# Kernel optimization log

Measured on AMD Instinct MI355X. Metric: run time of the kernel, lower is better.

## Reference

```python
import jax, jax.numpy as jnp
import numpy as np

B, S, D, H = 4, 2048, 1024, 16
HD = D // H


def setup_inputs() -> dict:
    key = jax.random.key(0)
    ks = jax.random.split(key, 12)
    s = 1.0 / np.sqrt(D)
    return {
        "query": jax.random.normal(ks[0], (B, S, D), jnp.float32),
        "key_": jax.random.normal(ks[1], (B, S, D), jnp.float32),
        "value": jax.random.normal(ks[2], (B, S, D), jnp.float32),
        "mask": jnp.ones((1, 1, S, S), dtype=bool),
        "Wq": jax.random.normal(ks[3], (D, D), jnp.float32) * s,
        "bq": jnp.zeros((D,), jnp.float32),
        "Wk": jax.random.normal(ks[4], (D, D), jnp.float32) * s,
        "bk": jnp.zeros((D,), jnp.float32),
        "Wv": jax.random.normal(ks[5], (D, D), jnp.float32) * s,
        "bv": jnp.zeros((D,), jnp.float32),
        "Wo": jax.random.normal(ks[6], (D, D), jnp.float32) * s,
        "bo": jnp.zeros((D,), jnp.float32),
    }


def reference(query, key_, value, mask, Wq, bq, Wk, bk, Wv, bv, Wo, bo):
    # Linear projections (torch Linear: x @ W^T + b; here W stored as (in, out))
    Q = query @ Wq + bq   # [B,S,D]
    K = key_ @ Wk + bk
    V = value @ Wv + bv
    # split heads -> [B,H,S,HD]
    Q = Q.reshape(B, S, H, HD).transpose(0, 2, 1, 3)
    K = K.reshape(B, S, H, HD).transpose(0, 2, 1, 3)
    V = V.reshape(B, S, H, HD).transpose(0, 2, 1, 3)
    scores = jnp.einsum("bhqd,bhkd->bhqk", Q, K) / jnp.sqrt(jnp.float32(HD))
    scores = jnp.where(mask, scores, jnp.float32(-jnp.inf))
    attn = jax.nn.softmax(scores, axis=-1)          # [B,H,S,S]
    ctx = jnp.einsum("bhqk,bhkd->bhqd", attn, V)    # dropout = identity (eval)
    ctx = ctx.transpose(0, 2, 1, 3).reshape(B, S, D)
    out = ctx @ Wo + bo
    return out, attn
```

## Files before the change

kernel.cpp:

```cpp
#include <hip/hip_runtime.h>

typedef __attribute__((ext_vector_type(4))) unsigned short u16x4;
typedef __attribute__((ext_vector_type(8))) short short8;
typedef __attribute__((ext_vector_type(4))) short short4b;
typedef __attribute__((ext_vector_type(4))) float f32x4;

__device__ inline unsigned short f2bf(float f) {
    union { float f; unsigned int i; } v; v.f = f;
    unsigned int r = v.i + 0x7fffu + ((v.i >> 16) & 1u);
    return (unsigned short)(r >> 16);
}

#define MFMA_PV(a, b, c) __builtin_amdgcn_mfma_f32_16x16x16bf16_1k((a), (b), (c), 0, 0, 0)
#define MFMA32(a, b, c) __builtin_amdgcn_mfma_f32_16x16x32_bf16((a), (b), (c), 0, 0, 0)

__device__ inline void gload_lds16(const unsigned short* g, unsigned short* l) {
    __builtin_amdgcn_global_load_lds(
        (const __attribute__((address_space(1))) void*)g,
        (__attribute__((address_space(3))) void*)l,
        16, 0, 0);
}

__global__ __launch_bounds__(256) void convert_f32_bf16(const float* __restrict__ in,
                                                        unsigned short* __restrict__ out,
                                                        int n4) {
    int i = blockIdx.x * 256 + threadIdx.x;
    if (i >= n4) return;
    float4 v = ((const float4*)in)[i];
    u16x4 o = { f2bf(v.x), f2bf(v.y), f2bf(v.z), f2bf(v.w) };
    ((u16x4*)out)[i] = o;
}

__global__ __launch_bounds__(256) void transpose_w4(const float* __restrict__ W0,
                                                    const float* __restrict__ W1,
                                                    const float* __restrict__ W2,
                                                    const float* __restrict__ W3,
                                                    unsigned short* __restrict__ O0,
                                                    unsigned short* __restrict__ O1,
                                                    unsigned short* __restrict__ O2,
                                                    unsigned short* __restrict__ O3) {
    __shared__ unsigned short tile[32][33];
    const float* in = (blockIdx.z == 0) ? W0 : (blockIdx.z == 1) ? W1
                    : (blockIdx.z == 2) ? W2 : W3;
    unsigned short* out = (blockIdx.z == 0) ? O0 : (blockIdx.z == 1) ? O1
                        : (blockIdx.z == 2) ? O2 : O3;
    int c0 = blockIdx.x * 32, r0 = blockIdx.y * 32;
    int x = threadIdx.x & 31, y = threadIdx.x >> 5;
#pragma unroll
    for (int i = 0; i < 4; i++)
        tile[y + i * 8][x] = f2bf(in[(size_t)(r0 + y + i * 8) * 1024 + c0 + x]);
    __syncthreads();
#pragma unroll
    for (int i = 0; i < 4; i++)
        out[(size_t)(c0 + y + i * 8) * 1024 + r0 + x] = tile[x][y + i * 8];
}

template <int F32OUT, int KTILED, int VTILED>
__global__ __launch_bounds__(256) void gemm_bt(const unsigned short* __restrict__ X,
                                               const unsigned short* __restrict__ Wt,
                                               const float* __restrict__ bias,
                                               void* __restrict__ outp,
                                               int M, int N, int K) {
    __shared__ unsigned short As[128 * 64];
    __shared__ unsigned short Bs[128 * 64];
    const int t = threadIdx.x;
    const int l = t & 63, w = t >> 6;
    const int lg = l >> 4, ln = l & 15;
    const int wm = (w >> 1) * 64, wn = (w & 1) * 64;
    const int m0 = blockIdx.y * 128, n0 = blockIdx.x * 128;

    const f32x4 zero = {0.f, 0.f, 0.f, 0.f};
    f32x4 acc[4][4];
#pragma unroll
    for (int i = 0; i < 4; i++)
#pragma unroll
        for (int j = 0; j < 4; j++) acc[i][j] = zero;

    int sr[4], sc[4];
#pragma unroll
    for (int i = 0; i < 4; i++) {
        int pos = i * 2048 + t * 8;
        sr[i] = pos >> 6;
        int c8 = (pos >> 3) & 7;
        sc[i] = (c8 ^ (sr[i] & 7)) * 8;
    }

    for (int k0 = 0; k0 < K; k0 += 64) {
#pragma unroll
        for (int i = 0; i < 4; i++)
            gload_lds16(&X[(size_t)(m0 + sr[i]) * K + k0 + sc[i]], &As[i * 2048 + w * 512]);
#pragma unroll
        for (int i = 0; i < 4; i++)
            gload_lds16(&Wt[(size_t)(n0 + sr[i]) * K + k0 + sc[i]], &Bs[i * 2048 + w * 512]);
        __syncthreads();
#pragma unroll
        for (int kk = 0; kk < 2; kk++) {
            short8 af[4], bfr[4];
#pragma unroll
            for (int i = 0; i < 4; i++) {
                int sl = (((kk << 2) | lg) ^ (ln & 7)) * 8;
                af[i]  = *(const short8*)&As[(wm + i * 16 + ln) * 64 + sl];
                bfr[i] = *(const short8*)&Bs[(wn + i * 16 + ln) * 64 + sl];
            }
#pragma unroll
            for (int i = 0; i < 4; i++)
#pragma unroll
                for (int j = 0; j < 4; j++)
                    acc[i][j] = MFMA32(af[i], bfr[j], acc[i][j]);
        }
        __syncthreads();
    }

#pragma unroll
    for (int j = 0; j < 4; j++) {
        int gn = n0 + wn + j * 16 + ln;
        float bvv = bias[gn];
#pragma unroll
        for (int i = 0; i < 4; i++) {
            int gm = m0 + wm + i * 16 + 4 * lg;
#pragma unroll
            for (int jj = 0; jj < 4; jj++) {
                float val = acc[i][j][jj] + bvv;
                int m = gm + jj, n = gn;
                if (F32OUT) {
                    __builtin_nontemporal_store(val, &((float*)outp)[(size_t)m * N + n]);
                } else if (KTILED) {
                    int b = m >> 11, s = m & 2047;
                    int itk = s >> 5, r = s & 31;
                    int h = n >> 6, dl = n & 63;
                    int cst = (dl >> 3) ^ (r & 7);
                    size_t off = (size_t)(b * 16 + h) * 131072 +
                                 (size_t)itk * 2048 + r * 64 + cst * 8 + (dl & 7);
                    ((unsigned short*)outp)[off] = f2bf(val);
                } else if (VTILED) {
                    int b = m >> 11, s = m & 2047;
                    int h = n >> 6, dl = n & 63;
                    size_t off = (size_t)(b * 16 + h) * 131072 +
                                 (size_t)(s >> 5) * 2048 + ((s >> 4) & 1) * 1024 +
                                 dl * 16 + (s & 15);
                    ((unsigned short*)outp)[off] = f2bf(val);
                } else {
                    ((unsigned short*)outp)[(size_t)m * N + n] = f2bf(val);
                }
            }
        }
    }
}

__global__ __launch_bounds__(256) void attn_pass1(const unsigned short* __restrict__ Qp,
                                                  const unsigned short* __restrict__ Kt,
                                                  float* __restrict__ se_buf) {
    const int S = 2048, Dm = 1024;
    __shared__ unsigned short Ks[2][4096];

    int blk = blockIdx.x;
    int wid = (blk & 7) * 128 + (blk >> 3);
    int qt = wid & 15, bh = wid >> 4;
    int b = bh >> 4, h = bh & 15;
    int t = threadIdx.x, l = t & 63, w = t >> 6;
    int lg = l >> 4, ln = l & 15;
    int qbase = qt * 128 + w * 16;

    const unsigned short* Qr0 = Qp + (size_t)(b * S + qbase + ln) * Dm + h * 64;
    const unsigned short* Qr1 = Qr0 + (size_t)64 * Dm;
    short8 q00 = *(const short8*)&Qr0[8 * lg];
    short8 q01 = *(const short8*)&Qr0[32 + 8 * lg];
    short8 q10 = *(const short8*)&Qr1[8 * lg];
    short8 q11 = *(const short8*)&Qr1[32 + 8 * lg];

    const unsigned short* Kb = Kt + (size_t)bh * 131072;
    const int c0x = (lg ^ (ln & 7)) * 8;
    const int c1x = ((4 + lg) ^ (ln & 7)) * 8;
    const int gb[4] = { ln * 64, 1024 + ln * 64, 2048 + ln * 64, 3072 + ln * 64 };

#define STAGE_K64(it, buf) do { \
    gload_lds16(Kb + (size_t)(it) * 4096 + t * 8, &Ks[buf][w * 512]); \
    gload_lds16(Kb + (size_t)(it) * 4096 + 2048 + t * 8, &Ks[buf][2048 + w * 512]); } while (0)

    const f32x4 zero = {0.f, 0.f, 0.f, 0.f};
    float se0 = 0.f, se1 = 0.f;
    int cur = 0;
    STAGE_K64(0, 0);
    __syncthreads();
    for (int it = 0; it < 32; ++it) {
        if (it < 31) STAGE_K64(it + 1, cur ^ 1);
        f32x4 s0[4], s1[4];
        __builtin_amdgcn_s_setprio(1);
#pragma unroll
        for (int g = 0; g < 4; g++) {
            short8 ka = *(const short8*)&Ks[cur][gb[g] + c0x];
            short8 kb = *(const short8*)&Ks[cur][gb[g] + c1x];
            s0[g] = MFMA32(ka, q00, zero);
            s0[g] = MFMA32(kb, q01, s0[g]);
            s1[g] = MFMA32(ka, q10, zero);
            s1[g] = MFMA32(kb, q11, s1[g]);
        }
        __builtin_amdgcn_s_setprio(0);
#pragma unroll
        for (int g = 0; g < 4; g++) {
#pragma unroll
            for (int j = 0; j < 4; j++) {
                se0 += __expf(s0[g][j] * 0.125f);
                se1 += __expf(s1[g][j] * 0.125f);
            }
        }
        __syncthreads();
        cur ^= 1;
    }
    se0 += __shfl_xor(se0, 16); se0 += __shfl_xor(se0, 32);
    se1 += __shfl_xor(se1, 16); se1 += __shfl_xor(se1, 32);
    if (lg == 0) {
        se_buf[bh * 2048 + qbase + ln] = se0;
        se_buf[bh * 2048 + qbase + 64 + ln] = se1;
    }
#undef STAGE_K64
}

__global__ __launch_bounds__(256) void attn_pass2(const unsigned short* __restrict__ Qp,
                                                  const unsigned short* __restrict__ Kt,
                                                  const unsigned short* __restrict__ Vt,
                                                  const float* __restrict__ se_buf,
                                                  float* __restrict__ attn_out,
                                                  unsigned short* __restrict__ Ctx) {
    const int S = 2048, Dm = 1024;
    __shared__ unsigned short Ks[2][4096];
    __shared__ unsigned short Vs[2][4096];

    int blk = blockIdx.x;
    int wid = (blk & 7) * 128 + (blk >> 3);
    int qt = wid & 15, bh = wid >> 4;
    int b = bh >> 4, h = bh & 15;
    int t = threadIdx.x, l = t & 63, w = t >> 6;
    int lg = l >> 4, ln = l & 15;
    int qbase = qt * 128 + w * 16;

    const unsigned short* Qr0 = Qp + (size_t)(b * S + qbase + ln) * Dm + h * 64;
    const unsigned short* Qr1 = Qr0 + (size_t)64 * Dm;
    short8 q00 = *(const short8*)&Qr0[8 * lg];
    short8 q01 = *(const short8*)&Qr0[32 + 8 * lg];
    short8 q10 = *(const short8*)&Qr1[8 * lg];
    short8 q11 = *(const short8*)&Qr1[32 + 8 * lg];

    float inv0 = 1.0f / se_buf[bh * 2048 + qbase + ln];
    float inv1 = 1.0f / se_buf[bh * 2048 + qbase + 64 + ln];

    const unsigned short* Kb = Kt + (size_t)bh * 131072;
    const unsigned short* Vb = Vt + (size_t)bh * 131072;
    const int c0x = (lg ^ (ln & 7)) * 8;
    const int c1x = ((4 + lg) ^ (ln & 7)) * 8;
    const int gb[4] = { ln * 64, 1024 + ln * 64, 2048 + ln * 64, 3072 + ln * 64 };

#define STAGE_K64(it, buf) do { \
    gload_lds16(Kb + (size_t)(it) * 4096 + t * 8, &Ks[buf][w * 512]); \
    gload_lds16(Kb + (size_t)(it) * 4096 + 2048 + t * 8, &Ks[buf][2048 + w * 512]); } while (0)
#define STAGE_V64(it, buf) do { \
    gload_lds16(Vb + (size_t)(it) * 4096 + t * 8, &Vs[buf][w * 512]); \
    gload_lds16(Vb + (size_t)(it) * 4096 + 2048 + t * 8, &Vs[buf][2048 + w * 512]); } while (0)

    const f32x4 zero = {0.f, 0.f, 0.f, 0.f};
    f32x4 acc0[4], acc1[4];
#pragma unroll
    for (int i = 0; i < 4; i++) { acc0[i] = zero; acc1[i] = zero; }

    float* Ar0 = attn_out + ((size_t)bh * S + qbase + ln) * S;
    float* Ar1 = Ar0 + (size_t)64 * S;

    int cur = 0;
    STAGE_K64(0, 0);
    STAGE_V64(0, 0);
    __syncthreads();
    for (int it = 0; it < 32; ++it) {
        if (it < 31) { STAGE_K64(it + 1, cur ^ 1); STAGE_V64(it + 1, cur ^ 1); }
        f32x4 s0[4], s1[4];
        __builtin_amdgcn_s_setprio(1);
#pragma unroll
        for (int g = 0; g < 4; g++) {
            short8 ka = *(const short8*)&Ks[cur][gb[g] + c0x];
            short8 kb = *(const short8*)&Ks[cur][gb[g] + c1x];
            s0[g] = MFMA32(ka, q00, zero);
            s0[g] = MFMA32(kb, q01, s0[g]);
            s1[g] = MFMA32(ka, q10, zero);
            s1[g] = MFMA32(kb, q11, s1[g]);
        }
        __builtin_amdgcn_s_setprio(0);

        union { short4b v; unsigned short u[4]; } pf0[4], pf1[4];
#pragma unroll
        for (int g = 0; g < 4; g++) {
            f32x4 pw0, pw1;
#pragma unroll
            for (int j = 0; j < 4; j++) {
                float p0 = __expf(s0[g][j] * 0.125f) * inv0;
                float p1 = __expf(s1[g][j] * 0.125f) * inv1;
                pw0[j] = p0; pf0[g].u[j] = f2bf(p0);
                pw1[j] = p1; pf1[g].u[j] = f2bf(p1);
            }
            __builtin_nontemporal_store(pw0, (f32x4*)&Ar0[it * 64 + g * 16 + 4 * lg]);
            __builtin_nontemporal_store(pw1, (f32x4*)&Ar1[it * 64 + g * 16 + 4 * lg]);
        }

        __builtin_amdgcn_s_setprio(1);
#pragma unroll
        for (int db = 0; db < 4; db++) {
            int vbase = (db * 16 + ln) * 16 + 4 * lg;
#pragma unroll
            for (int g = 0; g < 4; g++) {
                short4b vf = *(const short4b*)&Vs[cur][g * 1024 + vbase];
                acc0[db] = MFMA_PV(pf0[g].v, vf, acc0[db]);
                acc1[db] = MFMA_PV(pf1[g].v, vf, acc1[db]);
            }
        }
        __builtin_amdgcn_s_setprio(0);
        __syncthreads();
        cur ^= 1;
    }

#pragma unroll
    for (int db = 0; db < 4; db++)
#pragma unroll
        for (int j = 0; j < 4; j++) {
            Ctx[(size_t)(b * S + qbase + 4 * lg + j) * Dm + h * 64 + db * 16 + ln] =
                f2bf(acc0[db][j]);
            Ctx[(size_t)(b * S + qbase + 64 + 4 * lg + j) * Dm + h * 64 + db * 16 + ln] =
                f2bf(acc1[db][j]);
        }
#undef STAGE_K64
#undef STAGE_V64
}

extern "C" void kernel_launch(void* const* d_in, const int* in_sizes, int n_in,
                              void* d_out, int out_size, void* d_ws, size_t ws_size,
                              hipStream_t stream) {
    const float* query = (const float*)d_in[0];
    const float* key_  = (const float*)d_in[1];
    const float* value = (const float*)d_in[2];
    const float* Wq = (const float*)d_in[4];
    const float* bq = (const float*)d_in[5];
    const float* Wk = (const float*)d_in[6];
    const float* bk = (const float*)d_in[7];
    const float* Wv = (const float*)d_in[8];
    const float* bv = (const float*)d_in[9];
    const float* Wo = (const float*)d_in[10];
    const float* bo = (const float*)d_in[11];

    const size_t BSD = (size_t)4 * 2048 * 1024;
    const size_t DD  = (size_t)1024 * 1024;

    unsigned short* Xbuf = (unsigned short*)d_ws;
    unsigned short* Qp  = Xbuf + BSD;
    unsigned short* Kt  = Qp + BSD;
    unsigned short* Vt  = Kt + BSD;
    unsigned short* WqT = Vt + BSD;
    unsigned short* WkT = WqT + DD;
    unsigned short* WvT = WkT + DD;
    unsigned short* WoT = WvT + DD;
    float* SE = (float*)(WoT + DD);
    unsigned short* Ctx = Xbuf;

    float* out0 = (float*)d_out;
    float* attn = out0 + BSD;

    dim3 tb(256);
    int n4 = (int)(BSD / 4);
    dim3 cg((n4 + 255) / 256);

    transpose_w4<<<dim3(32, 32, 4), tb, 0, stream>>>(Wq, Wk, Wv, Wo, WqT, WkT, WvT, WoT);

    convert_f32_bf16<<<cg, tb, 0, stream>>>(query, Xbuf, n4);
    gemm_bt<0, 0, 0><<<dim3(8, 64), tb, 0, stream>>>(Xbuf, WqT, bq, Qp, 8192, 1024, 1024);

    convert_f32_bf16<<<cg, tb, 0, stream>>>(key_, Xbuf, n4);
    gemm_bt<0, 1, 0><<<dim3(8, 64), tb, 0, stream>>>(Xbuf, WkT, bk, Kt, 8192, 1024, 1024);

    attn_pass1<<<dim3(1024), tb, 0, stream>>>(Qp, Kt, SE);

    convert_f32_bf16<<<cg, tb, 0, stream>>>(value, Xbuf, n4);
    gemm_bt<0, 0, 1><<<dim3(8, 64), tb, 0, stream>>>(Xbuf, WvT, bv, Vt, 8192, 1024, 1024);

    attn_pass2<<<dim3(1024), tb, 0, stream>>>(Qp, Kt, Vt, SE, attn, Ctx);

    gemm_bt<1, 0, 0><<<dim3(8, 64), tb, 0, stream>>>(Ctx, WoT, bo, out0, 8192, 1024, 1024);
}
```

Baseline: 536.1 us.

## Merge launches: fused prep, batched Q/K GEMM, V-projection co-scheduled with pass1

Collapses the three input conversions and the weight transposes into a single prep launch. The Q and K projections now run as one batched GEMM grid. The V projection is co-launched in the same grid as attention pass1, so it overlaps the softmax-denominator pass. The goal is fewer launches and fewer serialization bubbles between small kernels. In exchange, three bf16 staging buffers are used instead of one, and the heterogeneous block roles share one LDS allocation. The exp is also rewritten as exp2f with a folded scale constant.

```diff
diff --git a/kernel.cpp b/kernel.cpp
--- a/kernel.cpp
+++ b/kernel.cpp
@@ -13,6 +13,8 @@
 
 #define MFMA_PV(a, b, c) __builtin_amdgcn_mfma_f32_16x16x16bf16_1k((a), (b), (c), 0, 0, 0)
 #define MFMA32(a, b, c) __builtin_amdgcn_mfma_f32_16x16x32_bf16((a), (b), (c), 0, 0, 0)
+
+#define SEXP(s) exp2f((s) * 0.18033688011112042f)
 
 __device__ inline void gload_lds16(const unsigned short* g, unsigned short* l) {
     __builtin_amdgcn_global_load_lds(
@@ -21,60 +23,54 @@
         16, 0, 0);
 }
 
-__global__ __launch_bounds__(256) void convert_f32_bf16(const float* __restrict__ in,
-                                                        unsigned short* __restrict__ out,
-                                                        int n4) {
-    int i = blockIdx.x * 256 + threadIdx.x;
-    if (i >= n4) return;
-    float4 v = ((const float4*)in)[i];
-    u16x4 o = { f2bf(v.x), f2bf(v.y), f2bf(v.z), f2bf(v.w) };
-    ((u16x4*)out)[i] = o;
-}
-
-__global__ __launch_bounds__(256) void transpose_w4(const float* __restrict__ W0,
-                                                    const float* __restrict__ W1,
-                                                    const float* __restrict__ W2,
-                                                    const float* __restrict__ W3,
-                                                    unsigned short* __restrict__ O0,
-                                                    unsigned short* __restrict__ O1,
-                                                    unsigned short* __restrict__ O2,
-                                                    unsigned short* __restrict__ O3) {
+__global__ __launch_bounds__(256) void prep(const float* __restrict__ q,
+                                            const float* __restrict__ k,
+                                            const float* __restrict__ v,
+                                            const float* __restrict__ W0,
+                                            const float* __restrict__ W1,
+                                            const float* __restrict__ W2,
+                                            const float* __restrict__ W3,
+                                            unsigned short* __restrict__ Xq,
+                                            unsigned short* __restrict__ Xk,
+                                            unsigned short* __restrict__ Xv,
+                                            unsigned short* __restrict__ O0,
+                                            unsigned short* __restrict__ O1,
+                                            unsigned short* __restrict__ O2,
+                                            unsigned short* __restrict__ O3) {
     __shared__ unsigned short tile[32][33];
-    const float* in = (blockIdx.z == 0) ? W0 : (blockIdx.z == 1) ? W1
-                    : (blockIdx.z == 2) ? W2 : W3;
-    unsigned short* out = (blockIdx.z == 0) ? O0 : (blockIdx.z == 1) ? O1
-                        : (blockIdx.z == 2) ? O2 : O3;
-    int c0 = blockIdx.x * 32, r0 = blockIdx.y * 32;
-    int x = threadIdx.x & 31, y = threadIdx.x >> 5;
-#pragma unroll
-    for (int i = 0; i < 4; i++)
-        tile[y + i * 8][x] = f2bf(in[(size_t)(r0 + y + i * 8) * 1024 + c0 + x]);
-    __syncthreads();
-#pragma unroll
-    for (int i = 0; i < 4; i++)
-        out[(size_t)(c0 + y + i * 8) * 1024 + r0 + x] = tile[x][y + i * 8];
-}
-
-template <int F32OUT, int KTILED, int VTILED>
-__global__ __launch_bounds__(256) void gemm_bt(const unsigned short* __restrict__ X,
-                                               const unsigned short* __restrict__ Wt,
-                                               const float* __restrict__ bias,
-                                               void* __restrict__ outp,
-                                               int M, int N, int K) {
-    __shared__ unsigned short As[128 * 64];
-    __shared__ unsigned short Bs[128 * 64];
+    int bid = blockIdx.x;
+    if (bid < 24576) {
+        const float* in = (bid < 8192) ? q : (bid < 16384) ? k : v;
+        unsigned short* out = (bid < 8192) ? Xq : (bid < 16384) ? Xk : Xv;
+        int i = (bid & 8191) * 256 + threadIdx.x;
+        float4 vv = ((const float4*)in)[i];
+        u16x4 o = { f2bf(vv.x), f2bf(vv.y), f2bf(vv.z), f2bf(vv.w) };
+        ((u16x4*)out)[i] = o;
+    } else {
+        int rem = bid - 24576;
+        int z = rem >> 10, idx = rem & 1023;
+        const float* in = (z == 0) ? W0 : (z == 1) ? W1 : (z == 2) ? W2 : W3;
+        unsigned short* out = (z == 0) ? O0 : (z == 1) ? O1 : (z == 2) ? O2 : O3;
+        int c0 = (idx & 31) * 32, r0 = (idx >> 5) * 32;
+        int x = threadIdx.x & 31, y = threadIdx.x >> 5;
+#pragma unroll
+        for (int i = 0; i < 4; i++)
+            tile[y + i * 8][x] = f2bf(in[(size_t)(r0 + y + i * 8) * 1024 + c0 + x]);
+        __syncthreads();
+#pragma unroll
+        for (int i = 0; i < 4; i++)
+            out[(size_t)(c0 + y + i * 8) * 1024 + r0 + x] = tile[x][y + i * 8];
+    }
+}
+
+__device__ __forceinline__ void gemm_core(const unsigned short* __restrict__ X,
+                                          const unsigned short* __restrict__ Wt,
+                                          unsigned short* As, unsigned short* Bs,
+                                          int m0, int n0, int K, f32x4 acc[4][4]) {
     const int t = threadIdx.x;
     const int l = t & 63, w = t >> 6;
     const int lg = l >> 4, ln = l & 15;
     const int wm = (w >> 1) * 64, wn = (w & 1) * 64;
-    const int m0 = blockIdx.y * 128, n0 = blockIdx.x * 128;
-
-    const f32x4 zero = {0.f, 0.f, 0.f, 0.f};
-    f32x4 acc[4][4];
-#pragma unroll
-    for (int i = 0; i < 4; i++)
-#pragma unroll
-        for (int j = 0; j < 4; j++) acc[i][j] = zero;
 
     int sr[4], sc[4];
 #pragma unroll
@@ -110,6 +106,35 @@
         }
         __syncthreads();
     }
+}
+
+__global__ __launch_bounds__(256) void gemm_qk(const unsigned short* __restrict__ Xq,
+                                               const unsigned short* __restrict__ Xk,
+                                               const unsigned short* __restrict__ WqT,
+                                               const unsigned short* __restrict__ WkT,
+                                               const float* __restrict__ bq,
+                                               const float* __restrict__ bk,
+                                               unsigned short* __restrict__ Qp,
+                                               unsigned short* __restrict__ Kt) {
+    __shared__ unsigned short As[8192];
+    __shared__ unsigned short Bs[8192];
+    const int z = blockIdx.z;
+    const unsigned short* X = z ? Xk : Xq;
+    const unsigned short* Wt = z ? WkT : WqT;
+    const float* bias = z ? bk : bq;
+    const int t = threadIdx.x, l = t & 63, w = t >> 6;
+    const int lg = l >> 4, ln = l & 15;
+    const int wm = (w >> 1) * 64, wn = (w & 1) * 64;
+    const int m0 = blockIdx.y * 128, n0 = blockIdx.x * 128;
+
+    const f32x4 zero = {0.f, 0.f, 0.f, 0.f};
+    f32x4 acc[4][4];
+#pragma unroll
+    for (int i = 0; i < 4; i++)
+#pragma unroll
+        for (int j = 0; j < 4; j++) acc[i][j] = zero;
+
+    gemm_core(X, Wt, As, Bs, m0, n0, 1024, acc);
 
 #pragma unroll
     for (int j = 0; j < 4; j++) {
@@ -122,43 +147,75 @@
             for (int jj = 0; jj < 4; jj++) {
                 float val = acc[i][j][jj] + bvv;
                 int m = gm + jj, n = gn;
-                if (F32OUT) {
-                    __builtin_nontemporal_store(val, &((float*)outp)[(size_t)m * N + n]);
-                } else if (KTILED) {
+                if (z) {
                     int b = m >> 11, s = m & 2047;
                     int itk = s >> 5, r = s & 31;
                     int h = n >> 6, dl = n & 63;
                     int cst = (dl >> 3) ^ (r & 7);
                     size_t off = (size_t)(b * 16 + h) * 131072 +
                                  (size_t)itk * 2048 + r * 64 + cst * 8 + (dl & 7);
-                    ((unsigned short*)outp)[off] = f2bf(val);
-                } else if (VTILED) {
+                    Kt[off] = f2bf(val);
+                } else {
+                    Qp[(size_t)m * 1024 + n] = f2bf(val);
+                }
+            }
+        }
+    }
+}
+
+__global__ __launch_bounds__(256) void gemmv_pass1(const unsigned short* __restrict__ Xv,
+                                                   const unsigned short* __restrict__ WvT,
+                                                   const float* __restrict__ bv,
+                                                   unsigned short* __restrict__ Vt,
+                                                   const unsigned short* __restrict__ Qp,
+                                                   const unsigned short* __restrict__ Kt,
+                                                   float* __restrict__ se_buf) {
+    const int S = 2048, Dm = 1024;
+    __shared__ unsigned short smem[16384];
+
+    int bid = blockIdx.x;
+    int t = threadIdx.x, l = t & 63, w = t >> 6;
+    int lg = l >> 4, ln = l & 15;
+
+    if (bid >= 1024) {
+        int g = bid - 1024;
+        const int wm = (w >> 1) * 64, wn = (w & 1) * 64;
+        const int m0 = (g >> 3) * 128, n0 = (g & 7) * 128;
+        const f32x4 zero = {0.f, 0.f, 0.f, 0.f};
+        f32x4 acc[4][4];
+#pragma unroll
+        for (int i = 0; i < 4; i++)
+#pragma unroll
+            for (int j = 0; j < 4; j++) acc[i][j] = zero;
+
+        gemm_core(Xv, WvT, smem, smem + 8192, m0, n0, 1024, acc);
+
+#pragma unroll
+        for (int j = 0; j < 4; j++) {
+            int gn = n0 + wn + j * 16 + ln;
+            float bvv = bv[gn];
+#pragma unroll
+            for (int i = 0; i < 4; i++) {
+                int gm = m0 + wm + i * 16 + 4 * lg;
+#pragma unroll
+                for (int jj = 0; jj < 4; jj++) {
+                    float val = acc[i][j][jj] + bvv;
+                    int m = gm + jj, n = gn;
                     int b = m >> 11, s = m & 2047;
                     int h = n >> 6, dl = n & 63;
                     size_t off = (size_t)(b * 16 + h) * 131072 +
                                  (size_t)(s >> 5) * 2048 + ((s >> 4) & 1) * 1024 +
                                  dl * 16 + (s & 15);
-                    ((unsigned short*)outp)[off] = f2bf(val);
-                } else {
-                    ((unsigned short*)outp)[(size_t)m * N + n] = f2bf(val);
+                    Vt[off] = f2bf(val);
                 }
             }
         }
-    }
-}
-
-__global__ __launch_bounds__(256) void attn_pass1(const unsigned short* __restrict__ Qp,
-                                                  const unsigned short* __restrict__ Kt,
-                                                  float* __restrict__ se_buf) {
-    const int S = 2048, Dm = 1024;
-    __shared__ unsigned short Ks[2][4096];
-
-    int blk = blockIdx.x;
-    int wid = (blk & 7) * 128 + (blk >> 3);
+        return;
+    }
+
+    int wid = (bid & 7) * 128 + (bid >> 3);
     int qt = wid & 15, bh = wid >> 4;
     int b = bh >> 4, h = bh & 15;
-    int t = threadIdx.x, l = t & 63, w = t >> 6;
-    int lg = l >> 4, ln = l & 15;
     int qbase = qt * 128 + w * 16;
 
     const unsigned short* Qr0 = Qp + (size_t)(b * S + qbase + ln) * Dm + h * 64;
@@ -174,8 +231,8 @@
     const int gb[4] = { ln * 64, 1024 + ln * 64, 2048 + ln * 64, 3072 + ln * 64 };
 
 #define STAGE_K64(it, buf) do { \
-    gload_lds16(Kb + (size_t)(it) * 4096 + t * 8, &Ks[buf][w * 512]); \
-    gload_lds16(Kb + (size_t)(it) * 4096 + 2048 + t * 8, &Ks[buf][2048 + w * 512]); } while (0)
+    gload_lds16(Kb + (size_t)(it) * 4096 + t * 8, &smem[(buf) * 4096 + w * 512]); \
+    gload_lds16(Kb + (size_t)(it) * 4096 + 2048 + t * 8, &smem[(buf) * 4096 + 2048 + w * 512]); } while (0)
 
     const f32x4 zero = {0.f, 0.f, 0.f, 0.f};
     float se0 = 0.f, se1 = 0.f;
@@ -188,8 +245,8 @@
         __builtin_amdgcn_s_setprio(1);
 #pragma unroll
         for (int g = 0; g < 4; g++) {
-            short8 ka = *(const short8*)&Ks[cur][gb[g] + c0x];
-            short8 kb = *(const short8*)&Ks[cur][gb[g] + c1x];
+            short8 ka = *(const short8*)&smem[cur * 4096 + gb[g] + c0x];
+            short8 kb = *(const short8*)&smem[cur * 4096 + gb[g] + c1x];
             s0[g] = MFMA32(ka, q00, zero);
             s0[g] = MFMA32(kb, q01, s0[g]);
             s1[g] = MFMA32(ka, q10, zero);
@@ -200,8 +257,8 @@
         for (int g = 0; g < 4; g++) {
 #pragma unroll
             for (int j = 0; j < 4; j++) {
-                se0 += __expf(s0[g][j] * 0.125f);
-                se1 += __expf(s1[g][j] * 0.125f);
+                se0 += SEXP(s0[g][j]);
+                se1 += SEXP(s1[g][j]);
             }
         }
         __syncthreads();
@@ -290,8 +347,8 @@
             f32x4 pw0, pw1;
 #pragma unroll
             for (int j = 0; j < 4; j++) {
-                float p0 = __expf(s0[g][j] * 0.125f) * inv0;
-                float p1 = __expf(s1[g][j] * 0.125f) * inv1;
+                float p0 = SEXP(s0[g][j]) * inv0;
+                float p1 = SEXP(s1[g][j]) * inv1;
                 pw0[j] = p0; pf0[g].u[j] = f2bf(p0);
                 pw1[j] = p1; pf1[g].u[j] = f2bf(p1);
             }
@@ -326,6 +383,41 @@
         }
 #undef STAGE_K64
 #undef STAGE_V64
+}
+
+__global__ __launch_bounds__(256) void gemm_out(const unsigned short* __restrict__ X,
+                                                const unsigned short* __restrict__ Wt,
+                                                const float* __restrict__ bias,
+                                                float* __restrict__ outp) {
+    __shared__ unsigned short As[8192];
+    __shared__ unsigned short Bs[8192];
+    const int t = threadIdx.x, l = t & 63, w = t >> 6;
+    const int lg = l >> 4, ln = l & 15;
+    const int wm = (w >> 1) * 64, wn = (w & 1) * 64;
+    const int m0 = blockIdx.y * 128, n0 = blockIdx.x * 128;
+
+    const f32x4 zero = {0.f, 0.f, 0.f, 0.f};
+    f32x4 acc[4][4];
+#pragma unroll
+    for (int i = 0; i < 4; i++)
+#pragma unroll
+        for (int j = 0; j < 4; j++) acc[i][j] = zero;
+
+    gemm_core(X, Wt, As, Bs, m0, n0, 1024, acc);
+
+#pragma unroll
+    for (int j = 0; j < 4; j++) {
+        int gn = n0 + wn + j * 16 + ln;
+        float bvv = bias[gn];
+#pragma unroll
+        for (int i = 0; i < 4; i++) {
+            int gm = m0 + wm + i * 16 + 4 * lg;
+#pragma unroll
+            for (int jj = 0; jj < 4; jj++)
+                __builtin_nontemporal_store(acc[i][j][jj] + bvv,
+                                            &outp[(size_t)(gm + jj) * 1024 + gn]);
+        }
+    }
 }
 
 extern "C" void kernel_launch(void* const* d_in, const int* in_sizes, int n_in,
@@ -346,8 +438,10 @@
     const size_t BSD = (size_t)4 * 2048 * 1024;
     const size_t DD  = (size_t)1024 * 1024;
 
-    unsigned short* Xbuf = (unsigned short*)d_ws;
-    unsigned short* Qp  = Xbuf + BSD;
+    unsigned short* Xq  = (unsigned short*)d_ws;
+    unsigned short* Xk  = Xq + BSD;
+    unsigned short* Xv  = Xk + BSD;
+    unsigned short* Qp  = Xv + BSD;
     unsigned short* Kt  = Qp + BSD;
     unsigned short* Vt  = Kt + BSD;
     unsigned short* WqT = Vt + BSD;
@@ -355,29 +449,21 @@
     unsigned short* WvT = WkT + DD;
     unsigned short* WoT = WvT + DD;
     float* SE = (float*)(WoT + DD);
-    unsigned short* Ctx = Xbuf;
+    unsigned short* Ctx = Xq;
 
     float* out0 = (float*)d_out;
     float* attn = out0 + BSD;
 
     dim3 tb(256);
-    int n4 = (int)(BSD / 4);
-    dim3 cg((n4 + 255) / 256);
-
-    transpose_w4<<<dim3(32, 32, 4), tb, 0, stream>>>(Wq, Wk, Wv, Wo, WqT, WkT, WvT, WoT);
-
-    convert_f32_bf16<<<cg, tb, 0, stream>>>(query, Xbuf, n4);
-    gemm_bt<0, 0, 0><<<dim3(8, 64), tb, 0, stream>>>(Xbuf, WqT, bq, Qp, 8192, 1024, 1024);
-
-    convert_f32_bf16<<<cg, tb, 0, stream>>>(key_, Xbuf, n4);
-    gemm_bt<0, 1, 0><<<dim3(8, 64), tb, 0, stream>>>(Xbuf, WkT, bk, Kt, 8192, 1024, 1024);
-
-    attn_pass1<<<dim3(1024), tb, 0, stream>>>(Qp, Kt, SE);
-
-    convert_f32_bf16<<<cg, tb, 0, stream>>>(value, Xbuf, n4);
-    gemm_bt<0, 0, 1><<<dim3(8, 64), tb, 0, stream>>>(Xbuf, WvT, bv, Vt, 8192, 1024, 1024);
+
+    prep<<<dim3(28672), tb, 0, stream>>>(query, key_, value, Wq, Wk, Wv, Wo,
+                                         Xq, Xk, Xv, WqT, WkT, WvT, WoT);
+
+    gemm_qk<<<dim3(8, 64, 2), tb, 0, stream>>>(Xq, Xk, WqT, WkT, bq, bk, Qp, Kt);
+
+    gemmv_pass1<<<dim3(1536), tb, 0, stream>>>(Xv, WvT, bv, Vt, Qp, Kt, SE);
 
     attn_pass2<<<dim3(1024), tb, 0, stream>>>(Qp, Kt, Vt, SE, attn, Ctx);
 
-    gemm_bt<1, 0, 0><<<dim3(8, 64), tb, 0, stream>>>(Ctx, WoT, bo, out0, 8192, 1024, 1024);
-}
+    gemm_out<<<dim3(8, 64), tb, 0, stream>>>(Ctx, WoT, bo, out0);
+}
```

Measured after the change: 556.6 us. 1.04x slower.

## Widen attention pass2 to 256 queries per block and use exp2 log-sum-exp

Applied to the files above, without the earlier changes.

attn_pass2 now handles four 64-row query groups per block instead of two, halving the grid. Each staged K/V tile is therefore reused across more queries, which cuts LDS staging traffic per output but raises register pressure. Softmax switches to exp2 with a precomputed log2 sum, folding scale, exponent and normalisation into one fma, and packs bf16 pairs with a hardware conversion. The host also converts all three inputs into separate buffers up front, and the GEMM is refactored into a shared core.

```diff
diff --git a/kernel.cpp b/kernel.cpp
--- a/kernel.cpp
+++ b/kernel.cpp
@@ -1,4 +1,5 @@
 #include <hip/hip_runtime.h>
+#include <hip/hip_bf16.h>
 
 typedef __attribute__((ext_vector_type(4))) unsigned short u16x4;
 typedef __attribute__((ext_vector_type(8))) short short8;
@@ -11,8 +12,16 @@
     return (unsigned short)(r >> 16);
 }
 
+__device__ inline unsigned int pk_bf16(float a, float b) {
+    union { __hip_bfloat162 h; unsigned int u; } cv;
+    cv.h = __float22bfloat162_rn(float2{a, b});
+    return cv.u;
+}
+
 #define MFMA_PV(a, b, c) __builtin_amdgcn_mfma_f32_16x16x16bf16_1k((a), (b), (c), 0, 0, 0)
 #define MFMA32(a, b, c) __builtin_amdgcn_mfma_f32_16x16x32_bf16((a), (b), (c), 0, 0, 0)
+
+#define SCL 0.18033688011112042f
 
 __device__ inline void gload_lds16(const unsigned short* g, unsigned short* l) {
     __builtin_amdgcn_global_load_lds(
@@ -55,26 +64,14 @@
         out[(size_t)(c0 + y + i * 8) * 1024 + r0 + x] = tile[x][y + i * 8];
 }
 
-template <int F32OUT, int KTILED, int VTILED>
-__global__ __launch_bounds__(256) void gemm_bt(const unsigned short* __restrict__ X,
-                                               const unsigned short* __restrict__ Wt,
-                                               const float* __restrict__ bias,
-                                               void* __restrict__ outp,
-                                               int M, int N, int K) {
-    __shared__ unsigned short As[128 * 64];
-    __shared__ unsigned short Bs[128 * 64];
+__device__ __forceinline__ void gemm_core(const unsigned short* __restrict__ X,
+                                          const unsigned short* __restrict__ Wt,
+                                          unsigned short* As, unsigned short* Bs,
+                                          int m0, int n0, int K, f32x4 acc[4][4]) {
     const int t = threadIdx.x;
     const int l = t & 63, w = t >> 6;
     const int lg = l >> 4, ln = l & 15;
     const int wm = (w >> 1) * 64, wn = (w & 1) * 64;
-    const int m0 = blockIdx.y * 128, n0 = blockIdx.x * 128;
-
-    const f32x4 zero = {0.f, 0.f, 0.f, 0.f};
-    f32x4 acc[4][4];
-#pragma unroll
-    for (int i = 0; i < 4; i++)
-#pragma unroll
-        for (int j = 0; j < 4; j++) acc[i][j] = zero;
 
     int sr[4], sc[4];
 #pragma unroll
@@ -110,6 +107,28 @@
         }
         __syncthreads();
     }
+}
+
+template <int MODE>
+__global__ __launch_bounds__(256) void gemm_proj(const unsigned short* __restrict__ X,
+                                                 const unsigned short* __restrict__ Wt,
+                                                 const float* __restrict__ bias,
+                                                 void* __restrict__ outp) {
+    __shared__ unsigned short As[8192];
+    __shared__ unsigned short Bs[8192];
+    const int t = threadIdx.x, l = t & 63, w = t >> 6;
+    const int lg = l >> 4, ln = l & 15;
+    const int wm = (w >> 1) * 64, wn = (w & 1) * 64;
+    const int m0 = blockIdx.y * 128, n0 = blockIdx.x * 128;
+
+    const f32x4 zero = {0.f, 0.f, 0.f, 0.f};
+    f32x4 acc[4][4];
+#pragma unroll
+    for (int i = 0; i < 4; i++)
+#pragma unroll
+        for (int j = 0; j < 4; j++) acc[i][j] = zero;
+
+    gemm_core(X, Wt, As, Bs, m0, n0, 1024, acc);
 
 #pragma unroll
     for (int j = 0; j < 4; j++) {
@@ -122,9 +141,9 @@
             for (int jj = 0; jj < 4; jj++) {
                 float val = acc[i][j][jj] + bvv;
                 int m = gm + jj, n = gn;
-                if (F32OUT) {
-                    __builtin_nontemporal_store(val, &((float*)outp)[(size_t)m * N + n]);
-                } else if (KTILED) {
+                if (MODE == 0) {
+                    ((unsigned short*)outp)[(size_t)m * 1024 + n] = f2bf(val);
+                } else if (MODE == 1) {
                     int b = m >> 11, s = m & 2047;
                     int itk = s >> 5, r = s & 31;
                     int h = n >> 6, dl = n & 63;
@@ -132,7 +151,7 @@
                     size_t off = (size_t)(b * 16 + h) * 131072 +
                                  (size_t)itk * 2048 + r * 64 + cst * 8 + (dl & 7);
                     ((unsigned short*)outp)[off] = f2bf(val);
-                } else if (VTILED) {
+                } else if (MODE == 2) {
                     int b = m >> 11, s = m & 2047;
                     int h = n >> 6, dl = n & 63;
                     size_t off = (size_t)(b * 16 + h) * 131072 +
@@ -140,7 +159,7 @@
                                  dl * 16 + (s & 15);
                     ((unsigned short*)outp)[off] = f2bf(val);
                 } else {
-                    ((unsigned short*)outp)[(size_t)m * N + n] = f2bf(val);
+                    __builtin_nontemporal_store(val, &((float*)outp)[(size_t)m * 1024 + n]);
                 }
             }
         }
@@ -149,7 +168,7 @@
 
 __global__ __launch_bounds__(256) void attn_pass1(const unsigned short* __restrict__ Qp,
                                                   const unsigned short* __restrict__ Kt,
-                                                  float* __restrict__ se_buf) {
+                                                  float* __restrict__ lse_buf) {
     const int S = 2048, Dm = 1024;
     __shared__ unsigned short Ks[2][4096];
 
@@ -200,8 +219,8 @@
         for (int g = 0; g < 4; g++) {
 #pragma unroll
             for (int j = 0; j < 4; j++) {
-                se0 += __expf(s0[g][j] * 0.125f);
-                se1 += __expf(s1[g][j] * 0.125f);
+                se0 += exp2f(s0[g][j] * SCL);
+                se1 += exp2f(s1[g][j] * SCL);
             }
         }
         __syncthreads();
@@ -210,8 +229,8 @@
     se0 += __shfl_xor(se0, 16); se0 += __shfl_xor(se0, 32);
     se1 += __shfl_xor(se1, 16); se1 += __shfl_xor(se1, 32);
     if (lg == 0) {
-        se_buf[bh * 2048 + qbase + ln] = se0;
-        se_buf[bh * 2048 + qbase + 64 + ln] = se1;
+        lse_buf[bh * 2048 + qbase + ln] = log2f(se0);
+        lse_buf[bh * 2048 + qbase + 64 + ln] = log2f(se1);
     }
 #undef STAGE_K64
 }
@@ -219,7 +238,7 @@
 __global__ __launch_bounds__(256) void attn_pass2(const unsigned short* __restrict__ Qp,
                                                   const unsigned short* __restrict__ Kt,
                                                   const unsigned short* __restrict__ Vt,
-                                                  const float* __restrict__ se_buf,
+                                                  const float* __restrict__ lse_buf,
                                                   float* __restrict__ attn_out,
                                                   unsigned short* __restrict__ Ctx) {
     const int S = 2048, Dm = 1024;
@@ -227,22 +246,24 @@
     __shared__ unsigned short Vs[2][4096];
 
     int blk = blockIdx.x;
-    int wid = (blk & 7) * 128 + (blk >> 3);
-    int qt = wid & 15, bh = wid >> 4;
+    int wid = (blk & 7) * 64 + (blk >> 3);
+    int qt = wid & 7, bh = wid >> 3;
     int b = bh >> 4, h = bh & 15;
     int t = threadIdx.x, l = t & 63, w = t >> 6;
     int lg = l >> 4, ln = l & 15;
-    int qbase = qt * 128 + w * 16;
-
-    const unsigned short* Qr0 = Qp + (size_t)(b * S + qbase + ln) * Dm + h * 64;
-    const unsigned short* Qr1 = Qr0 + (size_t)64 * Dm;
-    short8 q00 = *(const short8*)&Qr0[8 * lg];
-    short8 q01 = *(const short8*)&Qr0[32 + 8 * lg];
-    short8 q10 = *(const short8*)&Qr1[8 * lg];
-    short8 q11 = *(const short8*)&Qr1[32 + 8 * lg];
-
-    float inv0 = 1.0f / se_buf[bh * 2048 + qbase + ln];
-    float inv1 = 1.0f / se_buf[bh * 2048 + qbase + 64 + ln];
+    int qbase = qt * 256 + w * 16;
+
+    short8 qf[4][2];
+    float nlse[4];
+    float* Ar[4];
+    const unsigned short* Qr = Qp + (size_t)(b * S + qbase + ln) * Dm + h * 64;
+#pragma unroll
+    for (int u = 0; u < 4; u++) {
+        qf[u][0] = *(const short8*)&Qr[(size_t)u * 64 * Dm + 8 * lg];
+        qf[u][1] = *(const short8*)&Qr[(size_t)u * 64 * Dm + 32 + 8 * lg];
+        nlse[u] = -lse_buf[bh * 2048 + qbase + u * 64 + ln];
+        Ar[u] = attn_out + ((size_t)bh * S + qbase + u * 64 + ln) * S;
+    }
 
     const unsigned short* Kb = Kt + (size_t)bh * 131072;
     const unsigned short* Vb = Vt + (size_t)bh * 131072;
@@ -258,12 +279,11 @@
     gload_lds16(Vb + (size_t)(it) * 4096 + 2048 + t * 8, &Vs[buf][2048 + w * 512]); } while (0)
 
     const f32x4 zero = {0.f, 0.f, 0.f, 0.f};
-    f32x4 acc0[4], acc1[4];
-#pragma unroll
-    for (int i = 0; i < 4; i++) { acc0[i] = zero; acc1[i] = zero; }
-
-    float* Ar0 = attn_out + ((size_t)bh * S + qbase + ln) * S;
-    float* Ar1 = Ar0 + (size_t)64 * S;
+    f32x4 acc[4][4];
+#pragma unroll
+    for (int u = 0; u < 4; u++)
+#pragma unroll
+        for (int i = 0; i < 4; i++) acc[u][i] = zero;
 
     int cur = 0;
     STAGE_K64(0, 0);
@@ -271,32 +291,30 @@
     __syncthreads();
     for (int it = 0; it < 32; ++it) {
         if (it < 31) { STAGE_K64(it + 1, cur ^ 1); STAGE_V64(it + 1, cur ^ 1); }
-        f32x4 s0[4], s1[4];
-        __builtin_amdgcn_s_setprio(1);
+
+        union { short4b v; unsigned int u2[2]; } pf[4][4];
 #pragma unroll
         for (int g = 0; g < 4; g++) {
             short8 ka = *(const short8*)&Ks[cur][gb[g] + c0x];
             short8 kb = *(const short8*)&Ks[cur][gb[g] + c1x];
-            s0[g] = MFMA32(ka, q00, zero);
-            s0[g] = MFMA32(kb, q01, s0[g]);
-            s1[g] = MFMA32(ka, q10, zero);
-            s1[g] = MFMA32(kb, q11, s1[g]);
-        }
-        __builtin_amdgcn_s_setprio(0);
-
-        union { short4b v; unsigned short u[4]; } pf0[4], pf1[4];
-#pragma unroll
-        for (int g = 0; g < 4; g++) {
-            f32x4 pw0, pw1;
-#pragma unroll
-            for (int j = 0; j < 4; j++) {
-                float p0 = __expf(s0[g][j] * 0.125f) * inv0;
-                float p1 = __expf(s1[g][j] * 0.125f) * inv1;
-                pw0[j] = p0; pf0[g].u[j] = f2bf(p0);
-                pw1[j] = p1; pf1[g].u[j] = f2bf(p1);
-            }
-            __builtin_nontemporal_store(pw0, (f32x4*)&Ar0[it * 64 + g * 16 + 4 * lg]);
-            __builtin_nontemporal_store(pw1, (f32x4*)&Ar1[it * 64 + g * 16 + 4 * lg]);
+            f32x4 s[4];
+            __builtin_amdgcn_s_setprio(1);
+#pragma unroll
+            for (int u = 0; u < 4; u++) {
+                s[u] = MFMA32(ka, qf[u][0], zero);
+                s[u] = MFMA32(kb, qf[u][1], s[u]);
+            }
+            __builtin_amdgcn_s_setprio(0);
+#pragma unroll
+            for (int u = 0; u < 4; u++) {
+                f32x4 pw;
+#pragma unroll
+                for (int j = 0; j < 4; j++)
+                    pw[j] = exp2f(fmaf(s[u][j], SCL, nlse[u]));
+                pf[u][g].u2[0] = pk_bf16(pw[0], pw[1]);
+                pf[u][g].u2[1] = pk_bf16(pw[2], pw[3]);
+                __builtin_nontemporal_store(pw, (f32x4*)&Ar[u][it * 64 + g * 16 + 4 * lg]);
+            }
         }
 
         __builtin_amdgcn_s_setprio(1);
@@ -306,8 +324,9 @@
 #pragma unroll
             for (int g = 0; g < 4; g++) {
                 short4b vf = *(const short4b*)&Vs[cur][g * 1024 + vbase];
-                acc0[db] = MFMA_PV(pf0[g].v, vf, acc0[db]);
-                acc1[db] = MFMA_PV(pf1[g].v, vf, acc1[db]);
+#pragma unroll
+                for (int u = 0; u < 4; u++)
+                    acc[u][db] = MFMA_PV(pf[u][g].v, vf, acc[u][db]);
             }
         }
         __builtin_amdgcn_s_setprio(0);
@@ -316,14 +335,13 @@
     }
 
 #pragma unroll
-    for (int db = 0; db < 4; db++)
-#pragma unroll
-        for (int j = 0; j < 4; j++) {
-            Ctx[(size_t)(b * S + qbase + 4 * lg + j) * Dm + h * 64 + db * 16 + ln] =
-                f2bf(acc0[db][j]);
-            Ctx[(size_t)(b * S + qbase + 64 + 4 * lg + j) * Dm + h * 64 + db * 16 + ln] =
-                f2bf(acc1[db][j]);
-        }
+    for (int u = 0; u < 4; u++)
+#pragma unroll
+        for (int db = 0; db < 4; db++)
+#pragma unroll
+            for (int j = 0; j < 4; j++)
+                Ctx[(size_t)(b * S + qbase + u * 64 + 4 * lg + j) * Dm + h * 64 + db * 16 + ln] =
+                    f2bf(acc[u][db][j]);
 #undef STAGE_K64
 #undef STAGE_V64
 }
@@ -346,38 +364,38 @@
     const size_t BSD = (size_t)4 * 2048 * 1024;
     const size_t DD  = (size_t)1024 * 1024;
 
-    unsigned short* Xbuf = (unsigned short*)d_ws;
-    unsigned short* Qp  = Xbuf + BSD;
+    unsigned short* Xq  = (unsigned short*)d_ws;
+    unsigned short* Xk  = Xq + BSD;
+    unsigned short* Xv  = Xk + BSD;
+    unsigned short* Qp  = Xv + BSD;
     unsigned short* Kt  = Qp + BSD;
     unsigned short* Vt  = Kt + BSD;
     unsigned short* WqT = Vt + BSD;
     unsigned short* WkT = WqT + DD;
     unsigned short* WvT = WkT + DD;
     unsigned short* WoT = WvT + DD;
-    float* SE = (float*)(WoT + DD);
-    unsigned short* Ctx = Xbuf;
+    float* LSE = (float*)(WoT + DD);
+    unsigned short* Ctx = Xq;
 
     float* out0 = (float*)d_out;
     float* attn = out0 + BSD;
 
     dim3 tb(256);
-    int n4 = (int)(BSD / 4);
-    dim3 cg((n4 + 255) / 256);
-
+    dim3 cg(8192);
+
+    convert_f32_bf16<<<cg, tb, 0, stream>>>(query, Xq, (int)(BSD / 4));
+    convert_f32_bf16<<<cg, tb, 0, stream>>>(key_, Xk, (int)(BSD / 4));
+    convert_f32_bf16<<<cg, tb, 0, stream>>>(value, Xv, (int)(BSD / 4));
     transpose_w4<<<dim3(32, 32, 4), tb, 0, stream>>>(Wq, Wk, Wv, Wo, WqT, WkT, WvT, WoT);
 
-    convert_f32_bf16<<<cg, tb, 0, stream>>>(query, Xbuf, n4);
-    gemm_bt<0, 0, 0><<<dim3(8, 64), tb, 0, stream>>>(Xbuf, WqT, bq, Qp, 8192, 1024, 1024);
-
-    convert_f32_bf16<<<cg, tb, 0, stream>>>(key_, Xbuf, n4);
-    gemm_bt<0, 1, 0><<<dim3(8, 64), tb, 0, stream>>>(Xbuf, WkT, bk, Kt, 8192, 1024, 1024);
-
-    attn_pass1<<<dim3(1024), tb, 0, stream>>>(Qp, Kt, SE);
-
-    convert_f32_bf16<<<cg, tb, 0, stream>>>(value, Xbuf, n4);
-    gemm_bt<0, 0, 1><<<dim3(8, 64), tb, 0, stream>>>(Xbuf, WvT, bv, Vt, 8192, 1024, 1024);
-
-    attn_pass2<<<dim3(1024), tb, 0, stream>>>(Qp, Kt, Vt, SE, attn, Ctx);
-
-    gemm_bt<1, 0, 0><<<dim3(8, 64), tb, 0, stream>>>(Ctx, WoT, bo, out0, 8192, 1024, 1024);
-}
+    gemm_proj<0><<<dim3(8, 64), tb, 0, stream>>>(Xq, WqT, bq, Qp);
+    gemm_proj<1><<<dim3(8, 64), tb, 0, stream>>>(Xk, WkT, bk, Kt);
+
+    attn_pass1<<<dim3(1024), tb, 0, stream>>>(Qp, Kt, LSE);
+
+    gemm_proj<2><<<dim3(8, 64), tb, 0, stream>>>(Xv, WvT, bv, Vt);
+
+    attn_pass2<<<dim3(512), tb, 0, stream>>>(Qp, Kt, Vt, LSE, attn, Ctx);
+
+    gemm_proj<3><<<dim3(8, 64), tb, 0, stream>>>(Ctx, WoT, bo, out0);
+}
```

Result: slower. 571.2 us (+6.5%).
